# Kernel tuning notes

Hardware: AMD Instinct MI355X
Metric: run time of the kernel (lower is better)

Reference implementation:

```python
import jax, jax.numpy as jnp
import numpy as np
from jax import lax


def fps_indices(xyz, n_points):
    """Farthest point sampling. xyz: [B, N, 3]. Returns int32 indices [B, n_points].

    Classic PointNet++ algorithm: start from point 0, maintain per-point running
    min squared distance to the selected set, pick argmax each iteration.
    """
    B, N, _ = xyz.shape

    def step(carry, _):
        min_d, last_idx = carry  # min_d: [B, N], last_idx: [B]
        last_pt = jnp.take_along_axis(xyz, last_idx[:, None, None], axis=1)  # [B,1,3]
        d = jnp.sum((xyz - last_pt) ** 2, axis=-1)  # [B, N] squared dist to last pick
        min_d = jnp.minimum(min_d, d)
        nxt = jnp.argmax(min_d, axis=-1).astype(jnp.int32)  # [B]
        return (min_d, nxt), last_idx

    init = (jnp.full((B, N), jnp.inf, dtype=xyz.dtype), jnp.zeros((B,), jnp.int32))
    _, idxs = lax.scan(step, init, None, length=n_points)  # [n_points, B]
    return idxs.T  # [B, n_points]


def setup_inputs() -> dict:
    key = jax.random.key(0)
    k1, k2 = jax.random.split(key)
    B, C, N = 16, 128, 16384
    x = jax.random.normal(k1, (B, C, N), dtype=jnp.float32)
    x_xyz = jax.random.normal(k2, (B, 3, N), dtype=jnp.float32)
    return {"x": x, "x_xyz": x_xyz, "n_points": 4096}


def reference(x, x_xyz, n_points):
    # x: [B, C, N] features, x_xyz: [B, 3, N] coordinates (channels-first)
    xyz = jnp.transpose(x_xyz, (0, 2, 1))  # [B, N, 3]
    idx = fps_indices(xyz, n_points)  # [B, S] int32
    # Gather features and coordinates at sampled indices (channels-first output)
    x_s = jnp.take_along_axis(x, idx[:, None, :], axis=2)        # [B, C, S]
    xyz_s = jnp.take_along_axis(x_xyz, idx[:, None, :], axis=2)  # [B, 3, S]
    return x_s, xyz_s
```

## Files before the change

kernel.cpp:

```cpp
#include <hip/hip_runtime.h>
#include <hip/hip_bf16.h>

#pragma clang fp contract(off)

#define NTH   1024
#define PPT   16
#define NPTS  16384
#define BATCH 16
#define CFEAT 128
#define SMAX  4096
#define NWAVE (NTH / 64)
#define PRUNE_C 0.999995f

typedef __attribute__((ext_vector_type(2))) float f32x2;

__device__ __forceinline__ unsigned spread3(unsigned v) {
    v &= 0x3FFu;
    v = (v | (v << 16)) & 0x030000FFu;
    v = (v | (v << 8))  & 0x0300F00Fu;
    v = (v | (v << 4))  & 0x030C30C3u;
    v = (v | (v << 2))  & 0x09249249u;
    return v;
}
__device__ __forceinline__ unsigned qz10(float v) {
    int q = (int)((v + 6.0f) * (1023.0f / 12.0f));
    q = q < 0 ? 0 : (q > 1023 ? 1023 : q);
    return (unsigned)q;
}
__device__ __forceinline__ unsigned morton30(float x, float y, float z) {
    return (spread3(qz10(x)) << 2) | (spread3(qz10(y)) << 1) | spread3(qz10(z));
}

template <bool FUSED>
__global__ __launch_bounds__(NTH) void fps_kernel(const float* __restrict__ xyz,
                                                  const float* __restrict__ x,
                                                  int* __restrict__ idx_out,
                                                  float* __restrict__ out,
                                                  int S) {
    const int b    = blockIdx.x;
    const int tid  = threadIdx.x;
    const int wid  = tid >> 6;
    const int lane = tid & 63;
    const float* __restrict__ xb = xyz + (size_t)b * 3 * NPTS;

    __shared__ __align__(16) char s_pool[NPTS * sizeof(f32x2)];
    unsigned* s_ord = (unsigned*)s_pool;
    f32x2*    s_xy  = (f32x2*)s_pool;
    __shared__ unsigned s_hist[256];
    __shared__ unsigned long long s_slot[4];
    __shared__ int s_idx[SMAX];

    for (int i = tid; i < 256; i += NTH) s_hist[i] = 0;
    __syncthreads();
    for (int k = 0; k < PPT; ++k) {
        const int p = k * NTH + tid;
        const unsigned m = morton30(xb[p], xb[NPTS + p], xb[2 * NPTS + p]);
        atomicAdd(&s_hist[m >> 22], 1u);
    }
    __syncthreads();
    if (tid == 0) {
        unsigned acc = 0;
        for (int i = 0; i < 256; ++i) { const unsigned c = s_hist[i]; s_hist[i] = acc; acc += c; }
    }
    __syncthreads();
    for (int k = 0; k < PPT; ++k) {
        const int p = k * NTH + tid;
        const unsigned m = morton30(xb[p], xb[NPTS + p], xb[2 * NPTS + p]);
        const unsigned pos = atomicAdd(&s_hist[m >> 22], 1u);
        s_ord[pos] = (unsigned)p;
    }
    if (tid == 0) { s_slot[0] = s_slot[1] = s_slot[2] = s_slot[3] = 0ull; }
    __syncthreads();

    float Z[PPT], D[PPT];
    unsigned VI[PPT / 2];
#pragma unroll
    for (int k = 0; k < PPT; ++k) {
        const unsigned gi = s_ord[wid * (64 * PPT) + k * 64 + lane];
        if ((k & 1) == 0) VI[k >> 1] = gi;
        else              VI[k >> 1] |= (gi << 16);
        Z[k] = xb[2 * NPTS + gi];
        D[k] = INFINITY;
    }
    __syncthreads();

#pragma unroll
    for (int k = 0; k < PPT; ++k) {
        const int p = wid * (64 * PPT) + k * 64 + lane;
        const unsigned gi = (k & 1) ? (VI[k >> 1] >> 16) : (VI[k >> 1] & 0xFFFFu);
        f32x2 v;
        v.x = xb[gi];
        v.y = xb[NPTS + gi];
        s_xy[p] = v;
    }
    __syncthreads();

    float bxl =  INFINITY, byl =  INFINITY, bzl =  INFINITY;
    float bxh = -INFINITY, byh = -INFINITY, bzh = -INFINITY;
#pragma unroll
    for (int k = 0; k < PPT; ++k) {
        const f32x2 xy = s_xy[wid * (64 * PPT) + k * 64 + lane];
        bxl = fminf(bxl, xy.x); bxh = fmaxf(bxh, xy.x);
        byl = fminf(byl, xy.y); byh = fmaxf(byh, xy.y);
        bzl = fminf(bzl, Z[k]); bzh = fmaxf(bzh, Z[k]);
    }
#pragma unroll
    for (int off = 32; off >= 1; off >>= 1) {
        bxl = fminf(bxl, __shfl_xor(bxl, off)); bxh = fmaxf(bxh, __shfl_xor(bxh, off));
        byl = fminf(byl, __shfl_xor(byl, off)); byh = fmaxf(byh, __shfl_xor(byh, off));
        bzl = fminf(bzl, __shfl_xor(bzl, off)); bzh = fmaxf(bzh, __shfl_xor(bzh, off));
    }

    int   last  = 0;
    float px = xb[0], py = xb[NPTS], pz = xb[2 * NPTS];
    float wBest = INFINITY;
    unsigned long long myPack = 0;
    const int pbase = wid * (64 * PPT) + lane;

    for (int t = 0; t < S; ++t) {
        if (tid == 0) s_idx[t] = last;

        const float gx = fmaxf(fmaxf(bxl - px, px - bxh), 0.0f);
        const float gy = fmaxf(fmaxf(byl - py, py - byh), 0.0f);
        const float gz = fmaxf(fmaxf(bzl - pz, pz - bzh), 0.0f);
        const float lb = gx * gx + gy * gy + gz * gz;

        if (!(lb * PRUNE_C >= wBest)) {
            float    bestv = -INFINITY;
            unsigned bgg   = 0xFFFFu;
#pragma unroll
            for (int k = 0; k < PPT; ++k) {
                const f32x2 xy = s_xy[pbase + k * 64];
                const float dx = xy.x - px, dy = xy.y - py, dz = Z[k] - pz;
                const float d  = __builtin_fmaf(dz, dz, __builtin_fmaf(dx, dx, dy * dy));
                const float md = fminf(D[k], d);
                D[k] = md;
                const unsigned gg = (k & 1) ? (VI[k >> 1] >> 16)
                                            : (VI[k >> 1] & 0xFFFFu);
                if (md > bestv) { bestv = md; bgg = gg; }
            }
            const unsigned mybits = __float_as_uint(bestv);

            unsigned red = mybits;
#define DPP_MAX_STEP(CTRL)                                                     \
            {                                                                  \
                const unsigned tpp = (unsigned)__builtin_amdgcn_update_dpp(    \
                    0, (int)red, (CTRL), 0xf, 0xf, true);                      \
                red = (tpp > red) ? tpp : red;                                 \
            }
            DPP_MAX_STEP(0x111)
            DPP_MAX_STEP(0x112)
            DPP_MAX_STEP(0x114)
            DPP_MAX_STEP(0x118)
            DPP_MAX_STEP(0x142)
            DPP_MAX_STEP(0x143)
#undef DPP_MAX_STEP
            const unsigned bu = (unsigned)__builtin_amdgcn_readlane((int)red, 63);
            wBest = __uint_as_float(bu);

            myPack = 0;
            if (mybits == bu) {
                myPack = ((unsigned long long)mybits << 32)
                       | (unsigned long long)(0xFFFFFFFFu - bgg);
            }
        }
        if (myPack) atomicMax(&s_slot[t & 3], myPack);
        if (tid == 0) s_slot[(t + 2) & 3] = 0ull;
        __syncthreads();

        const unsigned long long win = s_slot[t & 3];
        last = (int)(0xFFFFFFFFu - (unsigned)(win & 0xFFFFFFFFull));
        px = xb[last]; py = xb[NPTS + last]; pz = xb[2 * NPTS + last];
    }

    __syncthreads();
    if (!FUSED) {
        for (int i = tid; i < S; i += NTH) idx_out[b * S + i] = s_idx[i];
    } else {
        for (int i = tid; i < CFEAT * S; i += NTH) {
            const int c = i / S, s = i - c * S;
            const long r = (long)b * CFEAT + c;
            out[r * S + s] = x[r * NPTS + s_idx[s]];
        }
        const long base2 = (long)BATCH * CFEAT * S;
        for (int i = tid; i < 3 * S; i += NTH) {
            const int c = i / S, s = i - c * S;
            const long r = (long)b * 3 + c;
            out[base2 + r * S + s] = xyz[r * NPTS + s_idx[s]];
        }
    }
}

__global__ void gather_kernel(const float* __restrict__ x,
                              const float* __restrict__ xyz,
                              const int* __restrict__ idx,
                              float* __restrict__ out,
                              int S) {
    const long nxs   = (long)BATCH * CFEAT * S;
    const long total = nxs + (long)BATCH * 3 * S;
    for (long i = (long)blockIdx.x * blockDim.x + threadIdx.x; i < total;
         i += (long)gridDim.x * blockDim.x) {
        if (i < nxs) {
            const int s  = (int)(i % S);
            const long r = i / S;
            const int b  = (int)(r / CFEAT);
            const int p  = idx[b * S + s];
            out[i] = x[r * NPTS + p];
        } else {
            const long j = i - nxs;
            const int s  = (int)(j % S);
            const long r = j / S;
            const int b  = (int)(r / 3);
            const int p  = idx[b * S + s];
            out[i] = xyz[r * NPTS + p];
        }
    }
}

extern "C" void kernel_launch(void* const* d_in, const int* in_sizes, int n_in,
                              void* d_out, int out_size, void* d_ws, size_t ws_size,
                              hipStream_t stream) {
    const float* x   = nullptr;
    const float* xyz = nullptr;
    for (int i = 0; i < n_in; ++i) {
        if (in_sizes[i] == BATCH * CFEAT * NPTS)  x   = (const float*)d_in[i];
        else if (in_sizes[i] == BATCH * 3 * NPTS) xyz = (const float*)d_in[i];
    }
    float* out = (float*)d_out;
    const int S = out_size / (BATCH * (CFEAT + 3));

    const size_t need = (size_t)BATCH * (size_t)S * sizeof(int);
    if (ws_size >= need && d_ws != nullptr) {
        int* idx = (int*)d_ws;
        fps_kernel<false><<<BATCH, NTH, 0, stream>>>(xyz, nullptr, idx, nullptr, S);
        gather_kernel<<<2048, 256, 0, stream>>>(x, xyz, idx, out, S);
    } else {
        fps_kernel<true><<<BATCH, NTH, 0, stream>>>(xyz, x, nullptr, out, S);
    }
}
```

Measured before the change: 4.138 ms.

## Split per-wave bounding box into two halves for finer FPS pruning

Each wave's 16 points per lane are now split into two 8-point groups, each with its own bounding box and cached wave maximum, so each half can be skipped independently when its lower bound cannot beat its current best. The inner loop tracks only the max value; the winning index is recovered afterwards by rescanning D in the lanes that hold the wave max, picking the smallest matching index. Bounds are made wave-uniform with readfirstlane. This adds register pressure (twelve box bounds and two cached maxima) and an extra rescan pass in exchange for fewer distance updates.

```diff
diff --git a/kernel.cpp b/kernel.cpp
--- a/kernel.cpp
+++ b/kernel.cpp
@@ -29,6 +29,27 @@
 }
 __device__ __forceinline__ unsigned morton30(float x, float y, float z) {
     return (spread3(qz10(x)) << 2) | (spread3(qz10(y)) << 1) | spread3(qz10(z));
+}
+__device__ __forceinline__ float rfl_f(float v) {
+    return __uint_as_float((unsigned)__builtin_amdgcn_readfirstlane(
+        (int)__float_as_uint(v)));
+}
+__device__ __forceinline__ unsigned wave_max_u32(unsigned v) {
+    unsigned red = v;
+#define DPP_MAX_STEP(CTRL)                                                     \
+    {                                                                          \
+        const unsigned tpp = (unsigned)__builtin_amdgcn_update_dpp(            \
+            0, (int)red, (CTRL), 0xf, 0xf, true);                              \
+        red = (tpp > red) ? tpp : red;                                         \
+    }
+    DPP_MAX_STEP(0x111)
+    DPP_MAX_STEP(0x112)
+    DPP_MAX_STEP(0x114)
+    DPP_MAX_STEP(0x118)
+    DPP_MAX_STEP(0x142)
+    DPP_MAX_STEP(0x143)
+#undef DPP_MAX_STEP
+    return (unsigned)__builtin_amdgcn_readlane((int)red, 63);
 }
 
 template <bool FUSED>
@@ -95,73 +116,104 @@
     }
     __syncthreads();
 
+    float axl =  INFINITY, ayl =  INFINITY, azl =  INFINITY;
+    float axh = -INFINITY, ayh = -INFINITY, azh = -INFINITY;
     float bxl =  INFINITY, byl =  INFINITY, bzl =  INFINITY;
     float bxh = -INFINITY, byh = -INFINITY, bzh = -INFINITY;
 #pragma unroll
     for (int k = 0; k < PPT; ++k) {
         const f32x2 xy = s_xy[wid * (64 * PPT) + k * 64 + lane];
-        bxl = fminf(bxl, xy.x); bxh = fmaxf(bxh, xy.x);
-        byl = fminf(byl, xy.y); byh = fmaxf(byh, xy.y);
-        bzl = fminf(bzl, Z[k]); bzh = fmaxf(bzh, Z[k]);
+        if (k < PPT / 2) {
+            axl = fminf(axl, xy.x); axh = fmaxf(axh, xy.x);
+            ayl = fminf(ayl, xy.y); ayh = fmaxf(ayh, xy.y);
+            azl = fminf(azl, Z[k]); azh = fmaxf(azh, Z[k]);
+        } else {
+            bxl = fminf(bxl, xy.x); bxh = fmaxf(bxh, xy.x);
+            byl = fminf(byl, xy.y); byh = fmaxf(byh, xy.y);
+            bzl = fminf(bzl, Z[k]); bzh = fmaxf(bzh, Z[k]);
+        }
     }
 #pragma unroll
     for (int off = 32; off >= 1; off >>= 1) {
+        axl = fminf(axl, __shfl_xor(axl, off)); axh = fmaxf(axh, __shfl_xor(axh, off));
+        ayl = fminf(ayl, __shfl_xor(ayl, off)); ayh = fmaxf(ayh, __shfl_xor(ayh, off));
+        azl = fminf(azl, __shfl_xor(azl, off)); azh = fmaxf(azh, __shfl_xor(azh, off));
         bxl = fminf(bxl, __shfl_xor(bxl, off)); bxh = fmaxf(bxh, __shfl_xor(bxh, off));
         byl = fminf(byl, __shfl_xor(byl, off)); byh = fmaxf(byh, __shfl_xor(byh, off));
         bzl = fminf(bzl, __shfl_xor(bzl, off)); bzh = fmaxf(bzh, __shfl_xor(bzh, off));
     }
-
-    int   last  = 0;
+    axl = rfl_f(axl); axh = rfl_f(axh); ayl = rfl_f(ayl); ayh = rfl_f(ayh);
+    azl = rfl_f(azl); azh = rfl_f(azh);
+    bxl = rfl_f(bxl); bxh = rfl_f(bxh); byl = rfl_f(byl); byh = rfl_f(byh);
+    bzl = rfl_f(bzl); bzh = rfl_f(bzh);
+
+    int   last = 0;
     float px = xb[0], py = xb[NPTS], pz = xb[2 * NPTS];
-    float wBest = INFINITY;
+    float bvA = -INFINITY, bvB = -INFINITY;
+    float wbA = INFINITY,  wbB = INFINITY;
     unsigned long long myPack = 0;
     const int pbase = wid * (64 * PPT) + lane;
 
     for (int t = 0; t < S; ++t) {
         if (tid == 0) s_idx[t] = last;
 
-        const float gx = fmaxf(fmaxf(bxl - px, px - bxh), 0.0f);
-        const float gy = fmaxf(fmaxf(byl - py, py - byh), 0.0f);
-        const float gz = fmaxf(fmaxf(bzl - pz, pz - bzh), 0.0f);
-        const float lb = gx * gx + gy * gy + gz * gz;
-
-        if (!(lb * PRUNE_C >= wBest)) {
-            float    bestv = -INFINITY;
-            unsigned bgg   = 0xFFFFu;
-#pragma unroll
-            for (int k = 0; k < PPT; ++k) {
+        const float gxa = fmaxf(fmaxf(axl - px, px - axh), 0.0f);
+        const float gya = fmaxf(fmaxf(ayl - py, py - ayh), 0.0f);
+        const float gza = fmaxf(fmaxf(azl - pz, pz - azh), 0.0f);
+        const float lbA = gxa * gxa + gya * gya + gza * gza;
+        const float gxb = fmaxf(fmaxf(bxl - px, px - bxh), 0.0f);
+        const float gyb = fmaxf(fmaxf(byl - py, py - byh), 0.0f);
+        const float gzb = fmaxf(fmaxf(bzl - pz, pz - bzh), 0.0f);
+        const float lbB = gxb * gxb + gyb * gyb + gzb * gzb;
+        const bool actA = !(lbA * PRUNE_C >= wbA);
+        const bool actB = !(lbB * PRUNE_C >= wbB);
+
+        if (actA) {
+            float bv = -INFINITY;
+#pragma unroll
+            for (int k = 0; k < PPT / 2; ++k) {
                 const f32x2 xy = s_xy[pbase + k * 64];
                 const float dx = xy.x - px, dy = xy.y - py, dz = Z[k] - pz;
                 const float d  = __builtin_fmaf(dz, dz, __builtin_fmaf(dx, dx, dy * dy));
                 const float md = fminf(D[k], d);
                 D[k] = md;
-                const unsigned gg = (k & 1) ? (VI[k >> 1] >> 16)
-                                            : (VI[k >> 1] & 0xFFFFu);
-                if (md > bestv) { bestv = md; bgg = gg; }
+                bv = fmaxf(bv, md);
             }
-            const unsigned mybits = __float_as_uint(bestv);
-
-            unsigned red = mybits;
-#define DPP_MAX_STEP(CTRL)                                                     \
-            {                                                                  \
-                const unsigned tpp = (unsigned)__builtin_amdgcn_update_dpp(    \
-                    0, (int)red, (CTRL), 0xf, 0xf, true);                      \
-                red = (tpp > red) ? tpp : red;                                 \
+            bvA = bv;
+            wbA = __uint_as_float(wave_max_u32(__float_as_uint(bv)));
+        }
+        if (actB) {
+            float bv = -INFINITY;
+#pragma unroll
+            for (int k = PPT / 2; k < PPT; ++k) {
+                const f32x2 xy = s_xy[pbase + k * 64];
+                const float dx = xy.x - px, dy = xy.y - py, dz = Z[k] - pz;
+                const float d  = __builtin_fmaf(dz, dz, __builtin_fmaf(dx, dx, dy * dy));
+                const float md = fminf(D[k], d);
+                D[k] = md;
+                bv = fmaxf(bv, md);
             }
-            DPP_MAX_STEP(0x111)
-            DPP_MAX_STEP(0x112)
-            DPP_MAX_STEP(0x114)
-            DPP_MAX_STEP(0x118)
-            DPP_MAX_STEP(0x142)
-            DPP_MAX_STEP(0x143)
-#undef DPP_MAX_STEP
-            const unsigned bu = (unsigned)__builtin_amdgcn_readlane((int)red, 63);
-            wBest = __uint_as_float(bu);
-
+            bvB = bv;
+            wbB = __uint_as_float(wave_max_u32(__float_as_uint(bv)));
+        }
+
+        if (actA || actB) {
+            const unsigned mybits = __float_as_uint(fmaxf(bvA, bvB));
+            const unsigned buA = __float_as_uint(wbA);
+            const unsigned buB = __float_as_uint(wbB);
+            const unsigned bu  = (buA > buB) ? buA : buB;
             myPack = 0;
             if (mybits == bu) {
+                unsigned mo = 0xFFFFFFFFu;
+#pragma unroll
+                for (int k = 0; k < PPT; ++k) {
+                    if (__float_as_uint(D[k]) == mybits) {
+                        const unsigned gg = (VI[k >> 1] >> ((k & 1) * 16)) & 0xFFFFu;
+                        mo = (gg < mo) ? gg : mo;
+                    }
+                }
                 myPack = ((unsigned long long)mybits << 32)
-                       | (unsigned long long)(0xFFFFFFFFu - bgg);
+                       | (unsigned long long)(0xFFFFFFFFu - mo);
             }
         }
         if (myPack) atomicMax(&s_slot[t & 3], myPack);
```

Measured after the change: 4.656 ms. 1.13x slower.
